# Kernel tuning notes

Measured on AMD Instinct MI355X. Metric: run time of the kernel, lower is better.

The kernel has to match this reference:

```python
import jax, jax.numpy as jnp
import numpy as np

N_HEAD = 16

def _rope_cache(dim, T):
    # matches precompute_rope_cache: angles = outer(pos, 1/theta^(2i/dim))
    pos = jnp.arange(T, dtype=jnp.float32)
    freq = 1.0 / (10000.0 ** (jnp.arange(0, dim, 2, dtype=jnp.float32) / dim))
    ang = pos[:, None] * freq[None, :]  # (T, dim//2)
    return jnp.cos(ang), jnp.sin(ang)

def _apply_rope(x, cos, sin):
    # x: (B, H, T, hs). Faithful to the (nonstandard, roll-based) torch apply_rope,
    # including the reassignment of x_rot before it is used for x_pass.
    x_rot, x_pass = x[..., ::2], x[..., 1::2]
    c = cos[None, None]  # (1,1,T,hs//2)
    s = sin[None, None]
    new_rot = x_rot * c - jnp.roll(x_pass, 1, axis=-1) * s
    new_pass = x_pass * c + jnp.roll(new_rot, -1, axis=-1) * s
    return jnp.stack([new_rot, new_pass], axis=-1).reshape(x.shape)

def setup_inputs() -> dict:
    key = jax.random.key(0)
    k1, k2, k3 = jax.random.split(key, 3)
    B, T, C = 2, 2048, 1024
    x = jax.random.normal(k1, (B, T, C), dtype=jnp.float32)
    w_attn = jax.random.normal(k2, (3 * C, C), dtype=jnp.float32) * 0.02
    w_proj = jax.random.normal(k3, (C, C), dtype=jnp.float32) * 0.02
    return {"x": x, "w_attn": w_attn, "w_proj": w_proj}

def reference(x, w_attn, w_proj):
    B, T, C = x.shape
    H = N_HEAD
    hs = C // H
    qkv = jnp.einsum('btc,dc->btd', x, w_attn)  # fused QKV projection (no bias)
    q, k, v = jnp.split(qkv, 3, axis=-1)
    def heads(t):
        return t.reshape(B, T, H, hs).transpose(0, 2, 1, 3)  # (B,H,T,hs)
    q, k, v = heads(q), heads(k), heads(v)
    cos, sin = _rope_cache(hs, T)
    q = _apply_rope(q, cos, sin)
    k = _apply_rope(k, cos, sin)
    scores = jnp.einsum('bhqd,bhkd->bhqk', q, k) / jnp.sqrt(jnp.float32(hs))
    causal = jnp.tril(jnp.ones((T, T), dtype=bool))
    scores = jnp.where(causal[None, None], scores, -jnp.inf)
    att = jax.nn.softmax(scores, axis=-1)
    y = jnp.einsum('bhqk,bhkd->bhqd', att, v)
    y = y.transpose(0, 2, 1, 3).reshape(B, T, C)
    return jnp.einsum('btc,dc->btd', y, w_proj)
```

## Files before the change

### kernel.cpp

```cpp
#include <hip/hip_runtime.h>

#define T_SEQ 2048
#define NHEAD 16
#define HS 64

typedef __bf16 bf16x8 __attribute__((ext_vector_type(8)));
typedef float f32x4 __attribute__((ext_vector_type(4)));

__device__ __forceinline__ unsigned short f2bf(float f) {
  union { float f; unsigned int u; } v; v.f = f;
  return (unsigned short)((v.u + 0x7fffu + ((v.u >> 16) & 1u)) >> 16);
}
__device__ __forceinline__ float bf2f(unsigned short h) {
  union { unsigned int u; float f; } v; v.u = ((unsigned int)h) << 16;
  return v.f;
}
__device__ __forceinline__ bf16x8 ld_bf8(const unsigned short* p) {
  return *(const bf16x8*)p;
}
__device__ __forceinline__ void st_bf8(unsigned short* p, bf16x8 v) {
  *(bf16x8*)p = v;
}
__device__ __forceinline__ bf16x8 cvt8(float4 a, float4 b) {
  bf16x8 r;
  r[0] = (__bf16)a.x; r[1] = (__bf16)a.y; r[2] = (__bf16)a.z; r[3] = (__bf16)a.w;
  r[4] = (__bf16)b.x; r[5] = (__bf16)b.y; r[6] = (__bf16)b.z; r[7] = (__bf16)b.w;
  return r;
}

__global__ __launch_bounds__(256, 2) void gemm_bt(
    const void* __restrict__ Av, const void* __restrict__ Bv,
    float* __restrict__ Cout,
    unsigned short* __restrict__ qb, unsigned short* __restrict__ kb,
    unsigned short* __restrict__ vtb,
    int M, int N, int K, int af32, int bf32, int mode) {
  __shared__ unsigned short As[128 * 64];
  __shared__ unsigned short Bs[128 * 64];
  const int tid = threadIdx.x;
  const int wid = tid >> 6, lane = tid & 63;
  const int quad = lane >> 4, l16 = lane & 15;
  const int m0 = blockIdx.y * 128, n0 = blockIdx.x * 128;
  const int wm = (wid >> 1) * 64, wn = (wid & 1) * 64;
  const int row_in = tid >> 3;
  const int col_in = (tid & 7) * 8;
  const float* Agf = (const float*)Av + (size_t)(m0 + row_in) * K + col_in;
  const float* Bgf = (const float*)Bv + (size_t)(n0 + row_in) * K + col_in;
  const unsigned short* Agh = (const unsigned short*)Av + (size_t)(m0 + row_in) * K + col_in;
  const unsigned short* Bgh = (const unsigned short*)Bv + (size_t)(n0 + row_in) * K + col_in;
  f32x4 acc[4][4] = {};
  const int nkt = K >> 6;
  for (int kt = 0; kt < nkt; ++kt) {
    bf16x8 as8[4], bs8[4];
    if (af32) {
      #pragma unroll
      for (int j = 0; j < 4; ++j) {
        const float* p = Agf + (size_t)j * 32 * K + kt * 64;
        as8[j] = cvt8(*(const float4*)p, *(const float4*)(p + 4));
      }
    } else {
      #pragma unroll
      for (int j = 0; j < 4; ++j)
        as8[j] = ld_bf8(Agh + (size_t)j * 32 * K + kt * 64);
    }
    if (bf32) {
      #pragma unroll
      for (int j = 0; j < 4; ++j) {
        const float* p = Bgf + (size_t)j * 32 * K + kt * 64;
        bs8[j] = cvt8(*(const float4*)p, *(const float4*)(p + 4));
      }
    } else {
      #pragma unroll
      for (int j = 0; j < 4; ++j)
        bs8[j] = ld_bf8(Bgh + (size_t)j * 32 * K + kt * 64);
    }
    __syncthreads();
    #pragma unroll
    for (int j = 0; j < 4; ++j) {
      st_bf8(&As[(j * 32 + row_in) * 64 + col_in], as8[j]);
      st_bf8(&Bs[(j * 32 + row_in) * 64 + col_in], bs8[j]);
    }
    __syncthreads();
    #pragma unroll
    for (int ks = 0; ks < 2; ++ks) {
      bf16x8 af[4], bfr[4];
      #pragma unroll
      for (int mt = 0; mt < 4; ++mt)
        af[mt] = ld_bf8(&As[(wm + mt * 16 + l16) * 64 + ks * 32 + quad * 8]);
      #pragma unroll
      for (int nt = 0; nt < 4; ++nt)
        bfr[nt] = ld_bf8(&Bs[(wn + nt * 16 + l16) * 64 + ks * 32 + quad * 8]);
      #pragma unroll
      for (int mt = 0; mt < 4; ++mt)
        #pragma unroll
        for (int nt = 0; nt < 4; ++nt)
          acc[mt][nt] = __builtin_amdgcn_mfma_f32_16x16x32_bf16(af[mt], bfr[nt], acc[mt][nt], 0, 0, 0);
    }
  }
  #pragma unroll
  for (int mt = 0; mt < 4; ++mt) {
    #pragma unroll
    for (int nt = 0; nt < 4; ++nt) {
      const int n = n0 + wn + nt * 16 + l16;
      #pragma unroll
      for (int r = 0; r < 4; ++r) {
        const int m = m0 + wm + mt * 16 + quad * 4 + r;
        if (mode == 0) {
          Cout[(size_t)m * N + n] = acc[mt][nt][r];
        } else {
          const unsigned short val = f2bf(acc[mt][nt][r]);
          const int b = m >> 11, t = m & (T_SEQ - 1);
          const int which = n >> 10, c = n & 1023;
          const int h = c >> 6, d = c & 63;
          const int bh = b * NHEAD + h;
          if (which == 0)      qb[((size_t)bh * T_SEQ + t) * HS + d] = val;
          else if (which == 1) kb[((size_t)bh * T_SEQ + t) * HS + d] = val;
          else                 vtb[((size_t)bh * HS + d) * T_SEQ + t] = val;
        }
      }
    }
  }
}

__global__ __launch_bounds__(256, 1) void rope(unsigned short* __restrict__ qb,
                                               unsigned short* __restrict__ kb) {
  const int idx = blockIdx.x * 256 + threadIdx.x;
  unsigned short* buf = (idx < 65536 ? qb : kb) + (size_t)(idx & 65535) * HS;
  const int t = idx & (T_SEQ - 1);
  float x[64];
  #pragma unroll
  for (int j = 0; j < 64; ++j) x[j] = bf2f(buf[j]);
  __asm__ volatile("" ::: "memory");
  float c[32], s[32], er[32];
  #pragma unroll
  for (int i = 0; i < 32; ++i) {
    const float ang = (float)t * exp2f(-0.41524101186092029f * (float)i);
    c[i] = cosf(ang); s[i] = sinf(ang);
  }
  #pragma unroll
  for (int i = 0; i < 32; ++i)
    er[i] = x[2 * i] * c[i] - x[(2 * i + 63) & 63] * s[i];
  #pragma unroll
  for (int i = 0; i < 32; ++i) {
    const float ep = x[2 * i + 1] * c[i] + er[(i + 1) & 31] * s[i];
    buf[2 * i]     = f2bf(er[i]);
    buf[2 * i + 1] = f2bf(ep);
  }
}

__global__ __launch_bounds__(64) void attn(
    const unsigned short* __restrict__ qb, const unsigned short* __restrict__ kb,
    const unsigned short* __restrict__ vt, unsigned short* __restrict__ yb) {
  __shared__ __bf16 Pl[16][72];
  const int u = blockIdx.x;
  const int qi = 127 - (u >> 5);
  const int bh = u & 31;
  const int q0 = qi * 16;
  const int lane = threadIdx.x & 63;
  const int quad = lane >> 4, l16 = lane & 15;

  const unsigned short* qptr = qb + ((size_t)bh * T_SEQ + q0 + l16) * HS;
  const bf16x8 aq0 = ld_bf8(qptr + quad * 8);
  const bf16x8 aq1 = ld_bf8(qptr + 32 + quad * 8);
  f32x4 O[4] = {};
  float m_i[4], l_i[4], alpha[4];
  #pragma unroll
  for (int r = 0; r < 4; ++r) { m_i[r] = -1e30f; l_i[r] = 0.f; }

  const unsigned short* kbase = kb + (size_t)bh * T_SEQ * HS;
  const unsigned short* vbase = vt + (size_t)bh * HS * T_SEQ;
  const int kend = q0 + 15;

  for (int k0 = 0; k0 <= kend; k0 += 64) {
    bf16x8 bk[4][2];
    #pragma unroll
    for (int t = 0; t < 4; ++t) {
      const unsigned short* kp = kbase + (size_t)(k0 + t * 16 + l16) * HS;
      bk[t][0] = ld_bf8(kp + quad * 8);
      bk[t][1] = ld_bf8(kp + 32 + quad * 8);
    }
    f32x4 S[4] = {};
    #pragma unroll
    for (int t = 0; t < 4; ++t) {
      S[t] = __builtin_amdgcn_mfma_f32_16x16x32_bf16(aq0, bk[t][0], S[t], 0, 0, 0);
      S[t] = __builtin_amdgcn_mfma_f32_16x16x32_bf16(aq1, bk[t][1], S[t], 0, 0, 0);
    }
    bf16x8 vb[2][4];
    #pragma unroll
    for (int c = 0; c < 2; ++c)
      #pragma unroll
      for (int vg = 0; vg < 4; ++vg)
        vb[c][vg] = ld_bf8(vbase + (size_t)(vg * 16 + l16) * T_SEQ + k0 + c * 32 + quad * 8);
    #pragma unroll
    for (int r = 0; r < 4; ++r) {
      const int row = q0 + quad * 4 + r;
      float s[4];
      #pragma unroll
      for (int t = 0; t < 4; ++t)
        s[t] = (k0 + t * 16 + l16 <= row) ? S[t][r] * 0.125f : -1e30f;
      float tm = fmaxf(fmaxf(s[0], s[1]), fmaxf(s[2], s[3]));
      #pragma unroll
      for (int off = 1; off < 16; off <<= 1) tm = fmaxf(tm, __shfl_xor(tm, off, 64));
      const float mnew = fmaxf(m_i[r], tm);
      alpha[r] = __expf(m_i[r] - mnew);
      unsigned short h[4];
      float rs = 0.f;
      #pragma unroll
      for (int t = 0; t < 4; ++t) {
        h[t] = f2bf(__expf(s[t] - mnew));
        rs += bf2f(h[t]);
      }
      #pragma unroll
      for (int off = 1; off < 16; off <<= 1) rs += __shfl_xor(rs, off, 64);
      l_i[r] = l_i[r] * alpha[r] + rs;
      m_i[r] = mnew;
      #pragma unroll
      for (int t = 0; t < 4; ++t)
        Pl[quad * 4 + r][t * 16 + l16] = __builtin_bit_cast(__bf16, h[t]);
    }
    #pragma unroll
    for (int vg = 0; vg < 4; ++vg)
      #pragma unroll
      for (int r = 0; r < 4; ++r) O[vg][r] *= alpha[r];
    #pragma unroll
    for (int c = 0; c < 2; ++c) {
      const bf16x8 pa = *(const bf16x8*)&Pl[l16][c * 32 + quad * 8];
      #pragma unroll
      for (int vg = 0; vg < 4; ++vg)
        O[vg] = __builtin_amdgcn_mfma_f32_16x16x32_bf16(pa, vb[c][vg], O[vg], 0, 0, 0);
    }
  }
  const int b = bh >> 4, h = bh & 15;
  #pragma unroll
  for (int r = 0; r < 4; ++r) {
    const float inv = 1.0f / fmaxf(l_i[r], 1e-30f);
    const int row = q0 + quad * 4 + r;
    #pragma unroll
    for (int vg = 0; vg < 4; ++vg)
      yb[((size_t)b * T_SEQ + row) * 1024 + h * HS + vg * 16 + l16] = f2bf(O[vg][r] * inv);
  }
}

extern "C" void kernel_launch(void* const* d_in, const int* in_sizes, int n_in,
                              void* d_out, int out_size, void* d_ws, size_t ws_size,
                              hipStream_t stream) {
  const float* x      = (const float*)d_in[0];
  const float* w_attn = (const float*)d_in[1];
  const float* w_proj = (const float*)d_in[2];
  float* out = (float*)d_out;
  unsigned short* qb = (unsigned short*)d_ws;
  unsigned short* kb = qb + (size_t)4194304;
  unsigned short* vt = kb + (size_t)4194304;
  unsigned short* yb = vt + (size_t)4194304;

  gemm_bt<<<dim3(24, 32), 256, 0, stream>>>(x, w_attn, nullptr, qb, kb, vt,
                                            4096, 3072, 1024, 1, 1, 1);
  rope<<<dim3(512), 256, 0, stream>>>(qb, kb);
  attn<<<dim3(4096), 64, 0, stream>>>(qb, kb, vt, yb);
  gemm_bt<<<dim3(8, 32), 256, 0, stream>>>(yb, w_proj, out, nullptr, nullptr, nullptr,
                                           4096, 1024, 1024, 0, 1, 0);
}
```

Baseline: 305.7 us.

## Pre-convert inputs to bf16, use direct global-to-LDS loads, pack attention waves

Adds a conversion kernel that turns x, and the weights when the workspace is large enough, into bf16 before the GEMMs. The GEMM A operand, and B when it is already bf16, is now fetched with global_load_lds directly into shared memory, replacing the register round-trip and adding a trailing barrier each k-step. The attention kernel packs four independent 64-thread waves into one 256-thread block with per-wave LDS buffers, and raises wave priority around its MFMA sections. This trades extra conversion launches and memory traffic for cheaper GEMM loads and fewer, larger attention blocks.

```diff
diff --git a/kernel.cpp b/kernel.cpp
--- a/kernel.cpp
+++ b/kernel.cpp
@@ -27,13 +27,26 @@
   r[4] = (__bf16)b.x; r[5] = (__bf16)b.y; r[6] = (__bf16)b.z; r[7] = (__bf16)b.w;
   return r;
 }
+__device__ __forceinline__ void gload_lds16(const void* g, void* l) {
+  __builtin_amdgcn_global_load_lds(
+      (const __attribute__((address_space(1))) unsigned int*)g,
+      (__attribute__((address_space(3))) unsigned int*)l, 16, 0, 0);
+}
+
+__global__ __launch_bounds__(256) void cvt_bf16(const float* __restrict__ src,
+                                                unsigned short* __restrict__ dst) {
+  const size_t i = ((size_t)blockIdx.x * 256 + threadIdx.x) * 8;
+  const float4 a = *(const float4*)(src + i);
+  const float4 b = *(const float4*)(src + i + 4);
+  st_bf8(dst + i, cvt8(a, b));
+}
 
 __global__ __launch_bounds__(256, 2) void gemm_bt(
-    const void* __restrict__ Av, const void* __restrict__ Bv,
+    const unsigned short* __restrict__ A, const void* __restrict__ Bv,
     float* __restrict__ Cout,
     unsigned short* __restrict__ qb, unsigned short* __restrict__ kb,
     unsigned short* __restrict__ vtb,
-    int M, int N, int K, int af32, int bf32, int mode) {
+    int M, int N, int K, int bf32, int mode) {
   __shared__ unsigned short As[128 * 64];
   __shared__ unsigned short Bs[128 * 64];
   const int tid = threadIdx.x;
@@ -41,43 +54,39 @@
   const int quad = lane >> 4, l16 = lane & 15;
   const int m0 = blockIdx.y * 128, n0 = blockIdx.x * 128;
   const int wm = (wid >> 1) * 64, wn = (wid & 1) * 64;
-  const int row_in = tid >> 3;
-  const int col_in = (tid & 7) * 8;
-  const float* Agf = (const float*)Av + (size_t)(m0 + row_in) * K + col_in;
-  const float* Bgf = (const float*)Bv + (size_t)(n0 + row_in) * K + col_in;
-  const unsigned short* Agh = (const unsigned short*)Av + (size_t)(m0 + row_in) * K + col_in;
-  const unsigned short* Bgh = (const unsigned short*)Bv + (size_t)(n0 + row_in) * K + col_in;
+  const int srow = lane >> 3;
+  const int scol = (lane & 7) * 8;
+  const int brow = tid >> 3;
+  const int bcol = (tid & 7) * 8;
+  const unsigned short* Bh = (const unsigned short*)Bv;
+  const float* Bf = (const float*)Bv;
   f32x4 acc[4][4] = {};
   const int nkt = K >> 6;
   for (int kt = 0; kt < nkt; ++kt) {
-    bf16x8 as8[4], bs8[4];
-    if (af32) {
+    const int k0 = kt * 64;
+    #pragma unroll
+    for (int j = 0; j < 4; ++j) {
+      const int rr = wid * 32 + j * 8 + srow;
+      gload_lds16(A + (size_t)(m0 + rr) * K + k0 + scol,
+                  &As[(wid * 32 + j * 8) * 64]);
+    }
+    if (bf32) {
+      bf16x8 bs8[4];
       #pragma unroll
       for (int j = 0; j < 4; ++j) {
-        const float* p = Agf + (size_t)j * 32 * K + kt * 64;
-        as8[j] = cvt8(*(const float4*)p, *(const float4*)(p + 4));
-      }
+        const float* p = Bf + (size_t)(n0 + j * 32 + brow) * K + k0 + bcol;
+        bs8[j] = cvt8(*(const float4*)p, *(const float4*)(p + 4));
+      }
+      #pragma unroll
+      for (int j = 0; j < 4; ++j)
+        st_bf8(&Bs[(j * 32 + brow) * 64 + bcol], bs8[j]);
     } else {
       #pragma unroll
-      for (int j = 0; j < 4; ++j)
-        as8[j] = ld_bf8(Agh + (size_t)j * 32 * K + kt * 64);
-    }
-    if (bf32) {
-      #pragma unroll
       for (int j = 0; j < 4; ++j) {
-        const float* p = Bgf + (size_t)j * 32 * K + kt * 64;
-        bs8[j] = cvt8(*(const float4*)p, *(const float4*)(p + 4));
-      }
-    } else {
-      #pragma unroll
-      for (int j = 0; j < 4; ++j)
-        bs8[j] = ld_bf8(Bgh + (size_t)j * 32 * K + kt * 64);
-    }
-    __syncthreads();
-    #pragma unroll
-    for (int j = 0; j < 4; ++j) {
-      st_bf8(&As[(j * 32 + row_in) * 64 + col_in], as8[j]);
-      st_bf8(&Bs[(j * 32 + row_in) * 64 + col_in], bs8[j]);
+        const int rr = wid * 32 + j * 8 + srow;
+        gload_lds16(Bh + (size_t)(n0 + rr) * K + k0 + scol,
+                    &Bs[(wid * 32 + j * 8) * 64]);
+      }
     }
     __syncthreads();
     #pragma unroll
@@ -95,6 +104,7 @@
         for (int nt = 0; nt < 4; ++nt)
           acc[mt][nt] = __builtin_amdgcn_mfma_f32_16x16x32_bf16(af[mt], bfr[nt], acc[mt][nt], 0, 0, 0);
     }
+    __syncthreads();
   }
   #pragma unroll
   for (int mt = 0; mt < 4; ++mt) {
@@ -147,11 +157,12 @@
   }
 }
 
-__global__ __launch_bounds__(64) void attn(
+__global__ __launch_bounds__(256) void attn(
     const unsigned short* __restrict__ qb, const unsigned short* __restrict__ kb,
     const unsigned short* __restrict__ vt, unsigned short* __restrict__ yb) {
-  __shared__ __bf16 Pl[16][72];
-  const int u = blockIdx.x;
+  __shared__ __bf16 Pl[4][16][72];
+  const int wid = threadIdx.x >> 6;
+  const int u = blockIdx.x * 4 + wid;
   const int qi = 127 - (u >> 5);
   const int bh = u & 31;
   const int q0 = qi * 16;
@@ -179,11 +190,13 @@
       bk[t][1] = ld_bf8(kp + 32 + quad * 8);
     }
     f32x4 S[4] = {};
+    __builtin_amdgcn_s_setprio(1);
     #pragma unroll
     for (int t = 0; t < 4; ++t) {
       S[t] = __builtin_amdgcn_mfma_f32_16x16x32_bf16(aq0, bk[t][0], S[t], 0, 0, 0);
       S[t] = __builtin_amdgcn_mfma_f32_16x16x32_bf16(aq1, bk[t][1], S[t], 0, 0, 0);
     }
+    __builtin_amdgcn_s_setprio(0);
     bf16x8 vb[2][4];
     #pragma unroll
     for (int c = 0; c < 2; ++c)
@@ -215,19 +228,21 @@
       m_i[r] = mnew;
       #pragma unroll
       for (int t = 0; t < 4; ++t)
-        Pl[quad * 4 + r][t * 16 + l16] = __builtin_bit_cast(__bf16, h[t]);
+        Pl[wid][quad * 4 + r][t * 16 + l16] = __builtin_bit_cast(__bf16, h[t]);
     }
     #pragma unroll
     for (int vg = 0; vg < 4; ++vg)
       #pragma unroll
       for (int r = 0; r < 4; ++r) O[vg][r] *= alpha[r];
+    __builtin_amdgcn_s_setprio(1);
     #pragma unroll
     for (int c = 0; c < 2; ++c) {
-      const bf16x8 pa = *(const bf16x8*)&Pl[l16][c * 32 + quad * 8];
+      const bf16x8 pa = *(const bf16x8*)&Pl[wid][l16][c * 32 + quad * 8];
       #pragma unroll
       for (int vg = 0; vg < 4; ++vg)
         O[vg] = __builtin_amdgcn_mfma_f32_16x16x32_bf16(pa, vb[c][vg], O[vg], 0, 0, 0);
     }
+    __builtin_amdgcn_s_setprio(0);
   }
   const int b = bh >> 4, h = bh & 15;
   #pragma unroll
@@ -251,11 +266,28 @@
   unsigned short* kb = qb + (size_t)4194304;
   unsigned short* vt = kb + (size_t)4194304;
   unsigned short* yb = vt + (size_t)4194304;
-
-  gemm_bt<<<dim3(24, 32), 256, 0, stream>>>(x, w_attn, nullptr, qb, kb, vt,
-                                            4096, 3072, 1024, 1, 1, 1);
+  unsigned short* xb = yb;
+  unsigned short* wab = yb + (size_t)4194304;
+  unsigned short* wpb = wab + (size_t)3145728;
+  const int big = ws_size >= (size_t)40 * 1024 * 1024;
+
+  cvt_bf16<<<dim3(2048), 256, 0, stream>>>(x, xb);
+  if (big) {
+    cvt_bf16<<<dim3(1536), 256, 0, stream>>>(w_attn, wab);
+    cvt_bf16<<<dim3(512), 256, 0, stream>>>(w_proj, wpb);
+  }
+  if (big)
+    gemm_bt<<<dim3(24, 32), 256, 0, stream>>>(xb, wab, nullptr, qb, kb, vt,
+                                              4096, 3072, 1024, 0, 1);
+  else
+    gemm_bt<<<dim3(24, 32), 256, 0, stream>>>(xb, w_attn, nullptr, qb, kb, vt,
+                                              4096, 3072, 1024, 1, 1);
   rope<<<dim3(512), 256, 0, stream>>>(qb, kb);
-  attn<<<dim3(4096), 64, 0, stream>>>(qb, kb, vt, yb);
-  gemm_bt<<<dim3(8, 32), 256, 0, stream>>>(yb, w_proj, out, nullptr, nullptr, nullptr,
-                                           4096, 1024, 1024, 0, 1, 0);
-}
+  attn<<<dim3(1024), 256, 0, stream>>>(qb, kb, vt, yb);
+  if (big)
+    gemm_bt<<<dim3(8, 32), 256, 0, stream>>>(yb, wpb, out, nullptr, nullptr, nullptr,
+                                             4096, 1024, 1024, 0, 0);
+  else
+    gemm_bt<<<dim3(8, 32), 256, 0, stream>>>(yb, w_proj, out, nullptr, nullptr, nullptr,
+                                             4096, 1024, 1024, 1, 0);
+}
```

Result: faster. 296.8 us (-2.9%).
